# Kernel optimization log

Hardware: AMD Instinct MI355X
Metric: run time of the kernel (lower is better)

The kernel has to match this reference:

```python
import jax, jax.numpy as jnp
import numpy as np

B, S, R, D, A, P = 64, 128, 8, 10000, 10, 256


def setup_inputs() -> dict:
    key = jax.random.key(0)
    ks = jax.random.split(key, 7)
    return {
        "atom_hvs": jax.random.normal(ks[0], (A, D), jnp.float32),
        "pos_hvs": jax.random.normal(ks[1], (S, D), jnp.float32),
        "closure_tag": jax.random.normal(ks[2], (D,), jnp.float32),
        "W": jax.random.normal(ks[3], (P, D), jnp.float32) / np.float32(np.sqrt(D)),
        "b": jax.random.normal(ks[4], (P,), jnp.float32) * 0.01,
        "token_mask": jnp.ones((B, S), jnp.float32),
        "ring_mask": jnp.ones((B, R), jnp.float32),
        "atom_idx": jax.random.randint(ks[5], (B, S), 0, A),
        "ring_pos": jax.random.randint(ks[6], (B, R, 2), 0, S),
    }


def reference(atom_hvs, pos_hvs, closure_tag, W, b, token_mask, ring_mask, atom_idx, ring_pos):
    # HRR bind = circular convolution -> pointwise multiply in rFFT domain.
    # Bundle = sum; by linearity we sum in the frequency domain and do a
    # single irfft per molecule (same math as per-token conv + add).
    d = atom_hvs.shape[-1]
    Fa = jnp.fft.rfft(atom_hvs, axis=-1)          # [A, F]
    Fp = jnp.fft.rfft(pos_hvs, axis=-1)           # [S, F]
    Fc = jnp.fft.rfft(closure_tag)                # [F]

    s = atom_idx.shape[1]
    tok = Fa[atom_idx] * Fp[None, :s, :]          # [B, S, F] gather+bind
    freq = jnp.sum(token_mask[..., None] * tok, axis=1)   # [B, F] bundle

    ring = Fp[ring_pos[..., 0]] * Fp[ring_pos[..., 1]] * Fc  # [B, R, F]
    freq = freq + jnp.sum(ring_mask[..., None] * ring, axis=1)

    mol_hv = jnp.fft.irfft(freq, n=d, axis=-1)    # [B, D]
    return mol_hv @ W.T + b                       # [B, proj_dim]
```

## Files before the change

### kernel.cpp

```cpp
#include <hip/hip_runtime.h>

#define PI2 6.28318530717958647692f

#define NSIG 139
#define FS   5120

__global__ __launch_bounds__(256) void k_fwd(
                     const float* __restrict__ atom, const float* __restrict__ pos,
                     const float* __restrict__ clo, float2* __restrict__ spec) {
  __shared__ float lds[10000];
  unsigned sig = blockIdx.x, q = blockIdx.y;
  unsigned k1base = q * 10u;
  unsigned nk1 = (k1base + 10u <= 51u) ? 10u : (51u - k1base);
  const float* xb = (sig < 128u) ? (pos + sig * 10000u)
                   : ((sig < 138u) ? (atom + (sig - 128u) * 10000u) : clo);
  int tid = threadIdx.x;

  {
    float* csA = lds;
    float* csB = lds + 2500;
    float* csG = lds + 5000;
    float* csH = lds + 7500;
    for (int t2 = tid; t2 < 625; t2 += 256) {
      const float* p = xb + (t2 / 25) * 100 + (t2 % 25) * 4;
      float4 x0 = *(const float4*)(p);
      float4 x1 = *(const float4*)(p + 2500);
      float4 x2 = *(const float4*)(p + 5000);
      float4 x3 = *(const float4*)(p + 7500);
      float4 A, B, G, H;
      A.x = (x0.x + x2.x) + (x1.x + x3.x);
      A.y = (x0.y + x2.y) + (x1.y + x3.y);
      A.z = (x0.z + x2.z) + (x1.z + x3.z);
      A.w = (x0.w + x2.w) + (x1.w + x3.w);
      B.x = (x0.x + x2.x) - (x1.x + x3.x);
      B.y = (x0.y + x2.y) - (x1.y + x3.y);
      B.z = (x0.z + x2.z) - (x1.z + x3.z);
      B.w = (x0.w + x2.w) - (x1.w + x3.w);
      G.x = x0.x - x2.x;  G.y = x0.y - x2.y;
      G.z = x0.z - x2.z;  G.w = x0.w - x2.w;
      H.x = x1.x - x3.x;  H.y = x1.y - x3.y;
      H.z = x1.z - x3.z;  H.w = x1.w - x3.w;
      *(float4*)(csA + t2 * 4) = A;
      *(float4*)(csB + t2 * 4) = B;
      *(float4*)(csG + t2 * 4) = G;
      *(float4*)(csH + t2 * 4) = H;
    }
  }
  __syncthreads();

  unsigned ntile1 = nk1 * 25u;
  unsigned k1l = tid / 25u, n2q = (unsigned)tid % 25u, n2 = n2q * 4u;
  bool have = (unsigned)tid < ntile1;
  unsigned k1 = k1base + k1l;
  float resA[8], resB[8];
  if (have) {
    float cth, sth;
    __sincosf(PI2 * (float)k1 * 0.01f, &sth, &cth);
    unsigned m = k1 & 3u;
    const float4* creP = (const float4*)((m == 0u) ? lds
                          : (m == 2u) ? (lds + 2500) : (lds + 5000)) + n2q;
    const float4* cimP = (const float4*)(lds + 7500) + n2q;
    float im_mul = (m == 1u) ? 1.0f : (m == 3u) ? -1.0f : 0.0f;
    float c = 1.0f, s = 0.0f;
    float ar[4] = {}, as[4] = {};
#pragma unroll 5
    for (int n1l = 0; n1l < 25; ++n1l) {
      float4 Cre = creP[n1l * 25];
      float4 Cim = cimP[n1l * 25];
      float se = im_mul * s, ce = im_mul * c;
      ar[0] += Cre.x * c - Cim.x * se;  as[0] += Cim.x * ce + Cre.x * s;
      ar[1] += Cre.y * c - Cim.y * se;  as[1] += Cim.y * ce + Cre.y * s;
      ar[2] += Cre.z * c - Cim.z * se;  as[2] += Cim.z * ce + Cre.z * s;
      ar[3] += Cre.w * c - Cim.w * se;  as[3] += Cim.w * ce + Cre.w * s;
      float cn = c * cth - s * sth;
      float sn = s * cth + c * sth;
      c = cn; s = sn;
    }
    unsigned rb = (100u - k1) % 100u;
#pragma unroll
    for (int j = 0; j < 4; ++j) {
      float swA, cwA, swB, cwB;
      __sincosf(PI2 * (float)((n2 + j) * k1) * 1e-4f, &swA, &cwA);
      __sincosf(PI2 * (float)((n2 + j) * rb) * 1e-4f, &swB, &cwB);
      resA[2 * j + 0] = ar[j] * cwA - as[j] * swA;
      resA[2 * j + 1] = -(as[j] * cwA + ar[j] * swA);
      resB[2 * j + 0] = ar[j] * cwB + as[j] * swB;
      resB[2 * j + 1] = as[j] * cwB - ar[j] * swB;
    }
  }
  __syncthreads();
  float* xs = lds;
  if (have) {
    float* pA = xs + k1l * 200u + n2 * 2u;
    float* pB = xs + (nk1 + k1l) * 200u + n2 * 2u;
    *(float4*)(pA + 0) = make_float4(resA[0], resA[1], resA[2], resA[3]);
    *(float4*)(pA + 4) = make_float4(resA[4], resA[5], resA[6], resA[7]);
    *(float4*)(pB + 0) = make_float4(resB[0], resB[1], resB[2], resB[3]);
    *(float4*)(pB + 4) = make_float4(resB[4], resB[5], resB[6], resB[7]);
  }
  __syncthreads();

  unsigned nrow = 2u * nk1;
  float* cse = lds + 4000;
  float* cso = lds + 6000;
  for (int t3 = tid; t3 < (int)(nrow * 25u); t3 += 256) {
    const float* br = xs + (t3 / 25) * 200;
    int n2l = t3 % 25;
    float2 b0 = *(const float2*)(br + 2 * n2l);
    float2 b1 = *(const float2*)(br + 2 * (25 + n2l));
    float2 b2 = *(const float2*)(br + 2 * (50 + n2l));
    float2 b3 = *(const float2*)(br + 2 * (75 + n2l));
    float4 e, o;
    e.x = (b0.x + b2.x) + (b1.x + b3.x);
    e.y = (b0.y + b2.y) + (b1.y + b3.y);
    e.z = (b0.x + b2.x) - (b1.x + b3.x);
    e.w = (b0.y + b2.y) - (b1.y + b3.y);
    o.x = b0.x - b2.x;
    o.y = b1.y - b3.y;
    o.z = b0.y - b2.y;
    o.w = b1.x - b3.x;
    *(float4*)(cse + t3 * 4) = e;
    *(float4*)(cso + t3 * 4) = o;
  }
  __syncthreads();

  unsigned ntile3 = nrow * 26u;
  for (unsigned t = tid; t < ntile3; t += 256u) {
    unsigned lr = t / 26u, k2 = (t % 26u) * 2u;
    unsigned gk1 = (lr < nk1) ? (k1base + lr) : ((100u - (k1base + (lr - nk1))) % 100u);
    float cthA, sthA, cthB, sthB;
    __sincosf(PI2 * (float)k2 * 0.01f, &sthA, &cthA);
    __sincosf(PI2 * (float)(k2 + 1) * 0.01f, &sthB, &cthB);
    bool hi = (k2 & 2u) != 0u;
    float sq = hi ? -1.0f : 1.0f;
    const float4* pe = (const float4*)(cse + lr * 100);
    const float4* po = (const float4*)(cso + lr * 100);
    float cA = 1.0f, sA = 0.0f, cB = 1.0f, sB = 0.0f;
    float reA = 0.f, imA = 0.f, reB = 0.f, imB = 0.f;
#pragma unroll 5
    for (int n2l = 0; n2l < 25; ++n2l) {
      float4 e = pe[n2l];
      float4 o = po[n2l];
      float car = hi ? e.z : e.x;
      float cai = hi ? e.w : e.y;
      float cbr = o.x + sq * o.y;
      float cbi = o.z - sq * o.w;
      reA += car * cA + cai * sA;  imA += cai * cA - car * sA;
      reB += cbr * cB + cbi * sB;  imB += cbi * cB - cbr * sB;
      float cA1 = cA * cthA - sA * sthA, sA1 = sA * cthA + cA * sthA;
      float cB1 = cB * cthB - sB * sthB, sB1 = sB * cthB + cB * sthB;
      cA = cA1; sA = sA1; cB = cB1; sB = sB1;
    }
    unsigned kA = gk1 + 100u * k2;
    unsigned kB = gk1 + 100u * (k2 + 1);
    if (kA <= 5000u) spec[sig * FS + kA] = make_float2(reA, imA);
    if (kB <= 5000u) spec[sig * FS + kB] = make_float2(reB, imB);
  }
}

__global__ __launch_bounds__(256) void k_mix(const float2* __restrict__ spec,
                      const float* __restrict__ tmask, const float* __restrict__ rmask,
                      const int* __restrict__ aidx, const int* __restrict__ rpos,
                      float2* __restrict__ G) {
  __shared__ float2 FaS[10][64];
  __shared__ float2 FcS[64];
  __shared__ float tmS[8][128];
  __shared__ int   aiS[8][128];
  __shared__ float rmS[8][8];
  __shared__ int   rpS[8][8][2];
  __shared__ float2 red[4][8][64];
  int tid = threadIdx.x;
  int kl = tid & 63, grp = tid >> 6;
  int k = blockIdx.x * 64 + kl;
  int kc = k > 5000 ? 5000 : k;
  int b0 = blockIdx.y * 8;
  for (int i = tid; i < 640; i += 256) {
    int a = i >> 6, kk = i & 63;
    int kg = blockIdx.x * 64 + kk; if (kg > 5000) kg = 5000;
    FaS[a][kk] = spec[(128 + a) * FS + kg];
  }
  if (tid < 64) FcS[tid] = spec[138 * FS + kc];
  for (int i = tid; i < 8 * 128; i += 256) {
    int bb = i >> 7, ss = i & 127;
    tmS[bb][ss] = tmask[(b0 + bb) * 128 + ss];
    aiS[bb][ss] = aidx[(b0 + bb) * 128 + ss];
  }
  if (tid < 64) {
    int bb = tid >> 3, rr = tid & 7;
    rmS[bb][rr] = rmask[(b0 + bb) * 8 + rr];
    rpS[bb][rr][0] = rpos[((b0 + bb) * 8 + rr) * 2 + 0];
    rpS[bb][rr][1] = rpos[((b0 + bb) * 8 + rr) * 2 + 1];
  }
  __syncthreads();
  float fr[8] = {}, fi[8] = {};
  int sbase = grp * 32;
#pragma unroll 4
  for (int si = 0; si < 32; ++si) {
    int s = sbase + si;
    float2 fp = spec[s * FS + kc];
#pragma unroll
    for (int b = 0; b < 8; ++b) {
      int a = aiS[b][s];
      float tm = tmS[b][s];
      float2 fa = FaS[a][kl];
      fr[b] += tm * (fa.x * fp.x - fa.y * fp.y);
      fi[b] += tm * (fa.x * fp.y + fa.y * fp.x);
    }
  }
  float2 fc = FcS[kl];
#pragma unroll
  for (int rr = 0; rr < 2; ++rr) {
    int r = grp * 2 + rr;
#pragma unroll
    for (int b = 0; b < 8; ++b) {
      int p0 = rpS[b][r][0], p1 = rpS[b][r][1];
      float rm = rmS[b][r];
      float2 f0 = spec[p0 * FS + kc];
      float2 f1 = spec[p1 * FS + kc];
      float tr = f0.x * f1.x - f0.y * f1.y;
      float ti = f0.x * f1.y + f0.y * f1.x;
      fr[b] += rm * (tr * fc.x - ti * fc.y);
      fi[b] += rm * (tr * fc.y + ti * fc.x);
    }
  }
#pragma unroll
  for (int b = 0; b < 8; ++b) red[grp][b][kl] = make_float2(fr[b], fi[b]);
  __syncthreads();
#pragma unroll
  for (int j = 0; j < 2; ++j) {
    int slot = j * 256 + tid;
    int b = slot >> 6, kk = slot & 63;
    int kg = blockIdx.x * 64 + kk;
    if (kg <= 5000) {
      float R = red[0][b][kk].x + red[1][b][kk].x + red[2][b][kk].x + red[3][b][kk].x;
      float I = red[0][b][kk].y + red[1][b][kk].y + red[2][b][kk].y + red[3][b][kk].y;
      if (kg == 0 || kg == 5000) I = 0.0f;
      G[(size_t)(b0 + b) * 10000 + kg] = make_float2(R, I);
      if (kg >= 1 && kg <= 4999)
        G[(size_t)(b0 + b) * 10000 + (10000 - kg)] = make_float2(R, -I);
    }
  }
}

__global__ __launch_bounds__(256) void k_i1(const float2* __restrict__ G,
                                            float2* __restrict__ Bi) {
  __shared__ float lds[10400];
  unsigned sig = blockIdx.x;
  const float* gp = (const float*)(G + sig * 10000u);
  int tid = threadIdx.x;
  float* c0v = lds;
  float* c2v = lds + 2600;
  float* cpr = lds + 5200;
  float* cqt = lds + 7800;
  for (int t2 = tid; t2 < 650; t2 += 256) {
    const float* p = gp + (t2 / 26) * 200 + (t2 % 26) * 4;
    float4 g0 = *(const float4*)(p);
    float4 g1 = *(const float4*)(p + 5000);
    float4 g2 = *(const float4*)(p + 10000);
    float4 g3 = *(const float4*)(p + 15000);
    float4 a, b, pr, qt;
    a.x = (g0.x + g2.x) + (g1.x + g3.x);
    a.y = (g0.y + g2.y) + (g1.y + g3.y);
    a.z = (g0.z + g2.z) + (g1.z + g3.z);
    a.w = (g0.w + g2.w) + (g1.w + g3.w);
    b.x = (g0.x + g2.x) - (g1.x + g3.x);
    b.y = (g0.y + g2.y) - (g1.y + g3.y);
    b.z = (g0.z + g2.z) - (g1.z + g3.z);
    b.w = (g0.w + g2.w) - (g1.w + g3.w);
    pr.x = g0.x - g2.x;  pr.y = g0.y - g2.y;
    pr.z = g0.z - g2.z;  pr.w = g0.w - g2.w;
    qt.x = g1.y - g3.y;  qt.y = g1.x - g3.x;
    qt.z = g1.w - g3.w;  qt.w = g1.z - g3.z;
    *(float4*)(c0v + t2 * 4) = a;
    *(float4*)(c2v + t2 * 4) = b;
    *(float4*)(cpr + t2 * 4) = pr;
    *(float4*)(cqt + t2 * 4) = qt;
  }
  __syncthreads();
  unsigned t = blockIdx.y * 256u + tid;
  if (t >= 1300u) return;
  unsigned m1 = t / 26u, n2p = t % 26u, n2 = n2p * 2u;
  float cth, sth;
  __sincosf(PI2 * (float)m1 * 0.01f, &sth, &cth);
  unsigned m = m1 & 3u;
  const float4* pe  = (const float4*)((m == 0u) ? c0v : (m == 2u) ? c2v : cpr) + n2p;
  const float4* pe2 = (const float4*)((m == 0u) ? c2v : (m == 2u) ? c0v : cpr) + n2p;
  const float4* pq  = (const float4*)cqt + n2p;
  float qmul = (m == 1u) ? -1.0f : (m == 3u) ? 1.0f : 0.0f;
  float qmul2 = -qmul;
  float c = 1.0f, s = 0.0f, sg = 1.0f;
  float reA = 0.f, imA = 0.f, reB = 0.f, imB = 0.f;
  float reA2 = 0.f, imA2 = 0.f, reB2 = 0.f, imB2 = 0.f;
#pragma unroll 5
  for (int n1l = 0; n1l < 25; ++n1l) {
    float4 ev = pe[n1l * 26];
    float4 e2 = pe2[n1l * 26];
    float4 qv = pq[n1l * 26];
    float gx = ev.x + qmul * qv.x,  gy = ev.y - qmul * qv.y;
    float gz = ev.z + qmul * qv.z,  gw = ev.w - qmul * qv.w;
    float hx = e2.x + qmul2 * qv.x, hy = e2.y - qmul2 * qv.y;
    float hz = e2.z + qmul2 * qv.z, hw = e2.w - qmul2 * qv.w;
    reA += gx * c - gy * s;  imA += gy * c + gx * s;
    reB += gz * c - gw * s;  imB += gw * c + gz * s;
    float cs = sg * c, ss = sg * s;
    reA2 += hx * cs - hy * ss;  imA2 += hy * cs + hx * ss;
    reB2 += hz * cs - hw * ss;  imB2 += hw * cs + hz * ss;
    float cn = c * cth - s * sth;
    float sn = s * cth + c * sth;
    c = cn; s = sn; sg = -sg;
  }
  float w0 = (n2 == 0u || n2 == 50u) ? 0.5f : 1.0f;
  float w1 = (n2 == 50u) ? 0.0f : 1.0f;
  {
    float sw0, cw0, sw1, cw1;
    __sincosf(PI2 * (float)(n2 * m1) * 1e-4f, &sw0, &cw0);
    __sincosf(PI2 * (float)((n2 + 1u) * m1) * 1e-4f, &sw1, &cw1);
    float4 outv;
    outv.x = (reA * cw0 - imA * sw0) * w0;
    outv.y = (imA * cw0 + reA * sw0) * w0;
    outv.z = (reB * cw1 - imB * sw1) * w1;
    outv.w = (imB * cw1 + reB * sw1) * w1;
    *(float4*)((float*)Bi + (sig * 5200u + m1 * 52u + n2) * 2) = outv;
  }
  {
    unsigned m1b = m1 + 50u;
    float sw0, cw0, sw1, cw1;
    __sincosf(PI2 * (float)(n2 * m1b) * 1e-4f, &sw0, &cw0);
    __sincosf(PI2 * (float)((n2 + 1u) * m1b) * 1e-4f, &sw1, &cw1);
    float4 outv;
    outv.x = (reA2 * cw0 - imA2 * sw0) * w0;
    outv.y = (imA2 * cw0 + reA2 * sw0) * w0;
    outv.z = (reB2 * cw1 - imB2 * sw1) * w1;
    outv.w = (imB2 * cw1 + reB2 * sw1) * w1;
    *(float4*)((float*)Bi + (sig * 5200u + m1b * 52u + n2) * 2) = outv;
  }
}

__global__ __launch_bounds__(256) void k_i2(const float2* __restrict__ Bi,
                                            float* __restrict__ mol) {
  unsigned sig = blockIdx.x, q = blockIdx.y;
  int tid = threadIdx.x;
  unsigned t = blockIdx.z * 256u + tid;
  if (t >= 625u) return;
  unsigned m1l = t / 25u;
  unsigned m2 = (t % 25u) * 2u;
  const float* bp = (const float*)Bi + sig * 10400u + q * 2600u + m1l * 104u;
  float cthA, sthA, cthB, sthB;
  __sincosf(PI2 * (float)m2 * 0.01f, &sthA, &cthA);
  __sincosf(PI2 * (float)(m2 + 1u) * 0.01f, &sthB, &cthB);
  float cA = 1.0f, sA = 0.0f, cB = 1.0f, sB = 0.0f;
  float r0e = 0.f, r0o = 0.f, r1e = 0.f, r1o = 0.f;
#pragma unroll 4
  for (int jj = 0; jj < 26; ++jj) {
    const float4 v0 = *(const float4*)(bp + 4 * jj);
    r0e += v0.x * cA - v0.y * sA;
    r1e += v0.x * cB - v0.y * sB;
    float cA1 = cA * cthA - sA * sthA, sA1 = sA * cthA + cA * sthA;
    float cB1 = cB * cthB - sB * sthB, sB1 = sB * cthB + cB * sthB;
    r0o += v0.z * cA1 - v0.w * sA1;
    r1o += v0.z * cB1 - v0.w * sB1;
    cA = cA1 * cthA - sA1 * sthA; sA = sA1 * cthA + cA1 * sthA;
    cB = cB1 * cthB - sB1 * sthB; sB = sB1 * cthB + cB1 * sthB;
  }
  unsigned m1 = q * 25u + m1l;
  float* mp = mol + sig * 10000u + m1;
  mp[100u * m2]          = (r0e + r0o) * 2e-4f;
  mp[100u * (m2 + 1u)]   = (r1e + r1o) * 2e-4f;
  mp[100u * (m2 + 50u)]  = (r0e - r0o) * 2e-4f;
  mp[100u * (m2 + 51u)]  = (r1e - r1o) * 2e-4f;
}

__global__ __launch_bounds__(512) void k_proj(const float* __restrict__ mol,
                                              const float* __restrict__ W,
                                              float* __restrict__ part) {
  __shared__ float molS[40 * 66];
  __shared__ float WS[40][258];
  int tid = threadIdx.x;
  int d0 = blockIdx.x * 40;
  for (int i = tid; i < 40 * 64; i += 512) {
    int b = i / 40, dl = i % 40;
    molS[dl * 66 + b] = mol[(size_t)b * 10000 + d0 + dl];
  }
  for (int i = tid; i < 40 * 256; i += 512) {
    int p = i / 40, dl = i % 40;
    WS[dl][p] = W[(size_t)p * 10000 + d0 + dl];
  }
  __syncthreads();
  int p0 = (tid & 127) * 2;
  int bh = (tid >> 7) * 16;
  float acc[2][16] = {};
#pragma unroll 4
  for (int dl = 0; dl < 40; ++dl) {
    const float2 wv = *(const float2*)(&WS[dl][p0]);
    const float2* m2p = (const float2*)(molS + dl * 66 + bh);
#pragma unroll
    for (int qq = 0; qq < 8; ++qq) {
      float2 mv = m2p[qq];
      acc[0][2 * qq + 0] += wv.x * mv.x;  acc[1][2 * qq + 0] += wv.y * mv.x;
      acc[0][2 * qq + 1] += wv.x * mv.y;  acc[1][2 * qq + 1] += wv.y * mv.y;
    }
  }
#pragma unroll
  for (int b = 0; b < 16; ++b)
    *(float2*)(part + (size_t)blockIdx.x * 16384 + (bh + b) * 256 + p0) =
        make_float2(acc[0][b], acc[1][b]);
}

__global__ __launch_bounds__(256) void k_red(const float* __restrict__ part,
                                             const float* __restrict__ bias,
                                             float* __restrict__ out) {
  __shared__ float red[4][64];
  int tid = threadIdx.x;
  int pl = tid & 63, cg = tid >> 6;
  int b = blockIdx.x;
  int p = blockIdx.y * 64 + pl;
  float acc = 0.0f;
#pragma unroll 8
  for (int ch = cg; ch < 250; ch += 4)
    acc += part[(size_t)ch * 16384 + b * 256 + p];
  red[cg][pl] = acc;
  __syncthreads();
  if (tid < 64)
    out[b * 256 + p] = red[0][pl] + red[1][pl] + red[2][pl] + red[3][pl] + bias[p];
}

extern "C" void kernel_launch(void* const* d_in, const int* in_sizes, int n_in,
                              void* d_out, int out_size, void* d_ws, size_t ws_size,
                              hipStream_t stream) {
  const float* atom  = (const float*)d_in[0];
  const float* pos   = (const float*)d_in[1];
  const float* clo   = (const float*)d_in[2];
  const float* W     = (const float*)d_in[3];
  const float* bias  = (const float*)d_in[4];
  const float* tmask = (const float*)d_in[5];
  const float* rmask = (const float*)d_in[6];
  const int*   aidx  = (const int*)d_in[7];
  const int*   rpos  = (const int*)d_in[8];
  float* out = (float*)d_out;

  char* ws = (char*)d_ws;
  size_t off = 0;
  auto alloc = [&](size_t n) { off = (off + 255) & ~(size_t)255; size_t o = off; off += n; return o; };
  char* regA   = ws + alloc(16777216);
  float2* Bi   = (float2*)regA;
  float*  part = (float*)regA;
  float2* spec = (float2*)(ws + alloc((size_t)NSIG * FS * 8));
  float2* G    = (float2*)(ws + alloc((size_t)64 * 10000 * 8));
  float*  mol  = (float*)(ws + alloc((size_t)64 * 10000 * 4));

  k_fwd<<<dim3(NSIG, 6), dim3(256), 0, stream>>>(atom, pos, clo, spec);
  k_mix<<<dim3(80, 8), dim3(256), 0, stream>>>(spec, tmask, rmask, aidx, rpos, G);
  k_i1<<<dim3(64, 6), dim3(256), 0, stream>>>(G, Bi);
  k_i2<<<dim3(64, 4, 3), dim3(256), 0, stream>>>(Bi, mol);
  k_proj<<<dim3(250), dim3(512), 0, stream>>>(mol, W, part);
  k_red<<<dim3(64, 4), dim3(256), 0, stream>>>(part, bias, out);
}
```

Measured before the change: 161.4 us.

## Stage inverse FFT output in LDS, retile projection, trim Nyquist tile in forward

```diff
diff --git a/kernel.cpp b/kernel.cpp
--- a/kernel.cpp
+++ b/kernel.cpp
@@ -124,9 +124,9 @@
   }
   __syncthreads();
 
-  unsigned ntile3 = nrow * 26u;
+  unsigned ntile3 = nrow * 25u;
   for (unsigned t = tid; t < ntile3; t += 256u) {
-    unsigned lr = t / 26u, k2 = (t % 26u) * 2u;
+    unsigned lr = t / 25u, k2 = (t % 25u) * 2u;
     unsigned gk1 = (lr < nk1) ? (k1base + lr) : ((100u - (k1base + (lr - nk1))) % 100u);
     float cthA, sthA, cthB, sthB;
     __sincosf(PI2 * (float)k2 * 0.01f, &sthA, &cthA);
@@ -152,9 +152,19 @@
       cA = cA1; sA = sA1; cB = cB1; sB = sB1;
     }
     unsigned kA = gk1 + 100u * k2;
-    unsigned kB = gk1 + 100u * (k2 + 1);
-    if (kA <= 5000u) spec[sig * FS + kA] = make_float2(reA, imA);
-    if (kB <= 5000u) spec[sig * FS + kB] = make_float2(reB, imB);
+    spec[sig * FS + kA] = make_float2(reA, imA);
+    spec[sig * FS + kA + 100u] = make_float2(reB, imB);
+  }
+  if (k1base == 0u && tid == 255) {
+    const float4* pe = (const float4*)(cse);
+    float c = 1.0f, re = 0.f, im = 0.f;
+#pragma unroll 5
+    for (int n2l = 0; n2l < 25; ++n2l) {
+      float4 e = pe[n2l];
+      re += e.z * c; im += e.w * c;
+      c = -c;
+    }
+    spec[sig * FS + 5000u] = make_float2(re, im);
   }
 }
 
@@ -336,74 +346,83 @@
   }
 }
 
-__global__ __launch_bounds__(256) void k_i2(const float2* __restrict__ Bi,
+__global__ __launch_bounds__(640) void k_i2(const float2* __restrict__ Bi,
                                             float* __restrict__ mol) {
+  __shared__ float ls[100 * 26];
   unsigned sig = blockIdx.x, q = blockIdx.y;
   int tid = threadIdx.x;
-  unsigned t = blockIdx.z * 256u + tid;
-  if (t >= 625u) return;
-  unsigned m1l = t / 25u;
-  unsigned m2 = (t % 25u) * 2u;
-  const float* bp = (const float*)Bi + sig * 10400u + q * 2600u + m1l * 104u;
-  float cthA, sthA, cthB, sthB;
-  __sincosf(PI2 * (float)m2 * 0.01f, &sthA, &cthA);
-  __sincosf(PI2 * (float)(m2 + 1u) * 0.01f, &sthB, &cthB);
-  float cA = 1.0f, sA = 0.0f, cB = 1.0f, sB = 0.0f;
-  float r0e = 0.f, r0o = 0.f, r1e = 0.f, r1o = 0.f;
+  if (tid < 625) {
+    unsigned m1l = (unsigned)tid / 25u;
+    unsigned m2 = ((unsigned)tid % 25u) * 2u;
+    const float* bp = (const float*)Bi + sig * 10400u + q * 2600u + m1l * 104u;
+    float cthA, sthA, cthB, sthB;
+    __sincosf(PI2 * (float)m2 * 0.01f, &sthA, &cthA);
+    __sincosf(PI2 * (float)(m2 + 1u) * 0.01f, &sthB, &cthB);
+    float cA = 1.0f, sA = 0.0f, cB = 1.0f, sB = 0.0f;
+    float r0e = 0.f, r0o = 0.f, r1e = 0.f, r1o = 0.f;
 #pragma unroll 4
-  for (int jj = 0; jj < 26; ++jj) {
-    const float4 v0 = *(const float4*)(bp + 4 * jj);
-    r0e += v0.x * cA - v0.y * sA;
-    r1e += v0.x * cB - v0.y * sB;
-    float cA1 = cA * cthA - sA * sthA, sA1 = sA * cthA + cA * sthA;
-    float cB1 = cB * cthB - sB * sthB, sB1 = sB * cthB + cB * sthB;
-    r0o += v0.z * cA1 - v0.w * sA1;
-    r1o += v0.z * cB1 - v0.w * sB1;
-    cA = cA1 * cthA - sA1 * sthA; sA = sA1 * cthA + cA1 * sthA;
-    cB = cB1 * cthB - sB1 * sthB; sB = sB1 * cthB + cB1 * sthB;
-  }
-  unsigned m1 = q * 25u + m1l;
-  float* mp = mol + sig * 10000u + m1;
-  mp[100u * m2]          = (r0e + r0o) * 2e-4f;
-  mp[100u * (m2 + 1u)]   = (r1e + r1o) * 2e-4f;
-  mp[100u * (m2 + 50u)]  = (r0e - r0o) * 2e-4f;
-  mp[100u * (m2 + 51u)]  = (r1e - r1o) * 2e-4f;
+    for (int jj = 0; jj < 26; ++jj) {
+      const float4 v0 = *(const float4*)(bp + 4 * jj);
+      r0e += v0.x * cA - v0.y * sA;
+      r1e += v0.x * cB - v0.y * sB;
+      float cA1 = cA * cthA - sA * sthA, sA1 = sA * cthA + cA * sthA;
+      float cB1 = cB * cthB - sB * sthB, sB1 = sB * cthB + cB * sthB;
+      r0o += v0.z * cA1 - v0.w * sA1;
+      r1o += v0.z * cB1 - v0.w * sB1;
+      cA = cA1 * cthA - sA1 * sthA; sA = sA1 * cthA + cA1 * sthA;
+      cB = cB1 * cthB - sB1 * sthB; sB = sB1 * cthB + cB1 * sthB;
+    }
+    ls[m2 * 26 + m1l]          = (r0e + r0o) * 2e-4f;
+    ls[(m2 + 1u) * 26 + m1l]   = (r1e + r1o) * 2e-4f;
+    ls[(m2 + 50u) * 26 + m1l]  = (r0e - r0o) * 2e-4f;
+    ls[(m2 + 51u) * 26 + m1l]  = (r1e - r1o) * 2e-4f;
+  }
+  __syncthreads();
+  float* mp = mol + sig * 10000u + q * 25u;
+  for (int i = tid; i < 2500; i += 640) {
+    int m2 = i / 25, m1l = i % 25;
+    mp[100 * m2 + m1l] = ls[m2 * 26 + m1l];
+  }
 }
 
 __global__ __launch_bounds__(512) void k_proj(const float* __restrict__ mol,
                                               const float* __restrict__ W,
                                               float* __restrict__ part) {
-  __shared__ float molS[40 * 66];
-  __shared__ float WS[40][258];
+  __shared__ float molS[40 * 68];
+  __shared__ float WS[40][260];
   int tid = threadIdx.x;
   int d0 = blockIdx.x * 40;
   for (int i = tid; i < 40 * 64; i += 512) {
     int b = i / 40, dl = i % 40;
-    molS[dl * 66 + b] = mol[(size_t)b * 10000 + d0 + dl];
+    molS[dl * 68 + b] = mol[(size_t)b * 10000 + d0 + dl];
   }
   for (int i = tid; i < 40 * 256; i += 512) {
     int p = i / 40, dl = i % 40;
     WS[dl][p] = W[(size_t)p * 10000 + d0 + dl];
   }
   __syncthreads();
-  int p0 = (tid & 127) * 2;
-  int bh = (tid >> 7) * 16;
-  float acc[2][16] = {};
+  int p0 = (tid & 63) * 4;
+  int bh = (tid >> 6) * 8;
+  float acc[4][8] = {};
 #pragma unroll 4
   for (int dl = 0; dl < 40; ++dl) {
-    const float2 wv = *(const float2*)(&WS[dl][p0]);
-    const float2* m2p = (const float2*)(molS + dl * 66 + bh);
-#pragma unroll
-    for (int qq = 0; qq < 8; ++qq) {
-      float2 mv = m2p[qq];
-      acc[0][2 * qq + 0] += wv.x * mv.x;  acc[1][2 * qq + 0] += wv.y * mv.x;
-      acc[0][2 * qq + 1] += wv.x * mv.y;  acc[1][2 * qq + 1] += wv.y * mv.y;
-    }
-  }
-#pragma unroll
-  for (int b = 0; b < 16; ++b)
-    *(float2*)(part + (size_t)blockIdx.x * 16384 + (bh + b) * 256 + p0) =
-        make_float2(acc[0][b], acc[1][b]);
+    const float4 wv = *(const float4*)(&WS[dl][p0]);
+    const float4 m0 = *(const float4*)(molS + dl * 68 + bh);
+    const float4 m1 = *(const float4*)(molS + dl * 68 + bh + 4);
+#pragma unroll
+    for (int j = 0; j < 4; ++j) {
+      float w = (j == 0) ? wv.x : (j == 1) ? wv.y : (j == 2) ? wv.z : wv.w;
+      acc[j][0] += w * m0.x;  acc[j][1] += w * m0.y;
+      acc[j][2] += w * m0.z;  acc[j][3] += w * m0.w;
+      acc[j][4] += w * m1.x;  acc[j][5] += w * m1.y;
+      acc[j][6] += w * m1.z;  acc[j][7] += w * m1.w;
+    }
+  }
+#pragma unroll
+  for (int b = 0; b < 8; ++b) {
+    float4 v = make_float4(acc[0][b], acc[1][b], acc[2][b], acc[3][b]);
+    *(float4*)(part + (size_t)blockIdx.x * 16384 + (bh + b) * 256 + p0) = v;
+  }
 }
 
 __global__ __launch_bounds__(256) void k_red(const float* __restrict__ part,
@@ -451,7 +470,7 @@
   k_fwd<<<dim3(NSIG, 6), dim3(256), 0, stream>>>(atom, pos, clo, spec);
   k_mix<<<dim3(80, 8), dim3(256), 0, stream>>>(spec, tmask, rmask, aidx, rpos, G);
   k_i1<<<dim3(64, 6), dim3(256), 0, stream>>>(G, Bi);
-  k_i2<<<dim3(64, 4, 3), dim3(256), 0, stream>>>(Bi, mol);
+  k_i2<<<dim3(64, 4), dim3(640), 0, stream>>>(Bi, mol);
   k_proj<<<dim3(250), dim3(512), 0, stream>>>(mol, W, part);
   k_red<<<dim3(64, 4), dim3(256), 0, stream>>>(part, bias, out);
 }
```

After: 158.6 us. About the same (-1.7%).
